# Kernel tuning notes

Hardware: AMD Instinct MI355X
Metric: run time of the kernel (lower is better)

## Reference

```python
import jax, jax.numpy as jnp
import numpy as np

OUT_FEATURES = 11008
IN_FEATURES = 4096
PACKED_LEN = OUT_FEATURES * IN_FEATURES // 4  # 4 ternary vals per byte, 2 bits each


def setup_inputs() -> dict:
    key = jax.random.key(0)
    k1, k2, k3 = jax.random.split(key, 3)
    x = jax.random.normal(k1, (4, 1024, IN_FEATURES), dtype=jnp.float32)
    packed_weight = jax.random.randint(k2, (PACKED_LEN,), 0, 256, dtype=jnp.int32)
    weight_scale = jax.random.uniform(k3, (1,), dtype=jnp.float32)
    return {"x": x, "packed_weight": packed_weight, "weight_scale": weight_scale}


def _dequantize_weight(packed_weight, weight_scale):
    shifts = jnp.arange(0, 8, 2, dtype=jnp.int32)          # [4]
    q = ((packed_weight[:, None] >> shifts) & 3) - 1        # [P, 4]
    q = q.reshape(OUT_FEATURES, IN_FEATURES).astype(jnp.float32)
    return q * weight_scale.reshape(())                      # dequantize


def reference(x, packed_weight, weight_scale):
    w = _dequantize_weight(packed_weight, weight_scale)      # [out, in]
    # F.linear: y = x @ w.T  (bias=False)
    return jnp.einsum('bsi,oi->bso', x, w)
```

## Files before the change

### kernel.cpp

```cpp
#include <hip/hip_runtime.h>
#include <hip/hip_bf16.h>

#define OUT_F 11008
#define IN_F  4096
#define M_DIM 4096

typedef __attribute__((ext_vector_type(8))) short bf16x8;
typedef __attribute__((ext_vector_type(4))) float f32x4;
typedef __attribute__((ext_vector_type(8))) unsigned short us8;

__device__ __forceinline__ unsigned short f2bf_rne(float f) {
    unsigned u = __builtin_bit_cast(unsigned, f);
    u += 0x7fffu + ((u >> 16) & 1u);
    return (unsigned short)(u >> 16);
}

__global__ void cvt_x_kernel(const float* __restrict__ x,
                             unsigned short* __restrict__ xb) {
    size_t i = ((size_t)blockIdx.x * blockDim.x + threadIdx.x) * 8;
    float4 a = *(const float4*)(x + i);
    float4 b = *(const float4*)(x + i + 4);
    us8 o;
    o[0] = f2bf_rne(a.x); o[1] = f2bf_rne(a.y);
    o[2] = f2bf_rne(a.z); o[3] = f2bf_rne(a.w);
    o[4] = f2bf_rne(b.x); o[5] = f2bf_rne(b.y);
    o[6] = f2bf_rne(b.z); o[7] = f2bf_rne(b.w);
    *(us8*)(xb + i) = o;
}

__global__ void unpack_w_kernel(const int* __restrict__ pw,
                                unsigned short* __restrict__ wb) {
    size_t i = (size_t)blockIdx.x * blockDim.x + threadIdx.x;
    int4 v = ((const int4*)pw)[i];
    const unsigned long long LUT = 0x40003F800000BF80ull;
    us8 o0, o1;
#pragma unroll
    for (int j = 0; j < 4; j++) {
        o0[j]     = (unsigned short)(LUT >> (((v.x >> (2 * j)) & 3) * 16));
        o0[4 + j] = (unsigned short)(LUT >> (((v.y >> (2 * j)) & 3) * 16));
        o1[j]     = (unsigned short)(LUT >> (((v.z >> (2 * j)) & 3) * 16));
        o1[4 + j] = (unsigned short)(LUT >> (((v.w >> (2 * j)) & 3) * 16));
    }
    ((us8*)wb)[i * 2]     = o0;
    ((us8*)wb)[i * 2 + 1] = o1;
}

__global__ __launch_bounds__(256) void gemm_kernel(
    const unsigned short* __restrict__ A,
    const unsigned short* __restrict__ B,
    float* __restrict__ C,
    const float* __restrict__ scale_ptr) {
    constexpr int K = IN_F;
    constexpr int N = OUT_F;
    constexpr int NB_N = 86;

    __shared__ unsigned short sA[128 * 32];
    __shared__ unsigned short sB[128 * 32];

    const int tid  = threadIdx.x;
    const int wave = tid >> 6;
    const int lane = tid & 63;

    const int lin = blockIdx.y * gridDim.x + blockIdx.x;
    const int grp = lin >> 8;
    const int rem = lin & 255;
    const int gw  = (grp * 8 + 8 <= NB_N) ? 8 : (NB_N - grp * 8);
    const int bn  = grp * 8 + rem % gw;
    const int bm  = rem / gw;

    const int wm = (wave >> 1) * 64;
    const int wn = (wave & 1) * 64;

    const int srow = lane >> 2;
    const int sseg = (lane & 3) ^ ((lane >> 3) & 3);
    const int scol = sseg * 8;

    const unsigned short* Ag = A + (size_t)bm * 128 * K;
    const unsigned short* Bg = B + (size_t)bn * 128 * K;

    f32x4 acc[4][4];
#pragma unroll
    for (int i = 0; i < 4; i++)
#pragma unroll
        for (int j = 0; j < 4; j++) acc[i][j] = (f32x4){0.f, 0.f, 0.f, 0.f};

    const int quad = lane >> 4;
    const int mrow = lane & 15;
    const int sw   = quad ^ ((mrow >> 1) & 3);

    for (int k0 = 0; k0 < K; k0 += 32) {
        __syncthreads();
#pragma unroll
        for (int c = 0; c < 2; c++) {
            const int chunk = wave * 2 + c;
            const int row = chunk * 16 + srow;
            __builtin_amdgcn_global_load_lds(
                (const __attribute__((address_space(1))) void*)(Ag + (size_t)row * K + k0 + scol),
                (__attribute__((address_space(3))) void*)(sA + chunk * 512),
                16, 0, 0);
        }
#pragma unroll
        for (int c = 0; c < 2; c++) {
            const int chunk = wave * 2 + c;
            const int row = chunk * 16 + srow;
            __builtin_amdgcn_global_load_lds(
                (const __attribute__((address_space(1))) void*)(Bg + (size_t)row * K + k0 + scol),
                (__attribute__((address_space(3))) void*)(sB + chunk * 512),
                16, 0, 0);
        }
        __syncthreads();

        bf16x8 af[4], bfg[4];
#pragma unroll
        for (int t = 0; t < 4; t++) {
            const int ra = wm + t * 16 + mrow;
            const int rb = wn + t * 16 + mrow;
            af[t]  = *(const bf16x8*)(sA + (ra * 4 + sw) * 8);
            bfg[t] = *(const bf16x8*)(sB + (rb * 4 + sw) * 8);
        }
#pragma unroll
        for (int i = 0; i < 4; i++)
#pragma unroll
            for (int j = 0; j < 4; j++)
                acc[i][j] = __builtin_amdgcn_mfma_f32_16x16x32_bf16(
                    af[i], bfg[j], acc[i][j], 0, 0, 0);
    }

    const float scale = *scale_ptr;
    float* Cg = C + (size_t)bm * 128 * N + (size_t)bn * 128;
#pragma unroll
    for (int i = 0; i < 4; i++) {
#pragma unroll
        for (int j = 0; j < 4; j++) {
#pragma unroll
            for (int r = 0; r < 4; r++) {
                const int row = wm + i * 16 + quad * 4 + r;
                const int col = wn + j * 16 + mrow;
                Cg[(size_t)row * N + col] = acc[i][j][r] * scale;
            }
        }
    }
}

extern "C" void kernel_launch(void* const* d_in, const int* in_sizes, int n_in,
                              void* d_out, int out_size, void* d_ws, size_t ws_size,
                              hipStream_t stream) {
    const float* x   = (const float*)d_in[0];
    const int* pw    = (const int*)d_in[1];
    const float* wsc = (const float*)d_in[2];

    float* out = (float*)d_out;

    unsigned short* xb = (unsigned short*)d_ws;
    unsigned short* wb = (unsigned short*)((char*)d_ws + (size_t)M_DIM * IN_F * 2);

    cvt_x_kernel<<<8192, 256, 0, stream>>>(x, xb);

    unpack_w_kernel<<<11008, 256, 0, stream>>>(pw, wb);

    gemm_kernel<<<dim3(86, 32), 256, 0, stream>>>(xb, wb, out, wsc);
}
```

Measured before the change: 675.5 us.

## Use 256x256 tiles with double-buffered LDS pipeline and XCD-aware block mapping

Rewrites the GEMM to use 256x256 block tiles with 8 waves (each 128x64), a K step of 64 split into two 32-wide halves, and double-buffered LDS. Global-to-LDS prefetch of the next tile is interleaved with MFMA phases through explicit vmcnt/lgkmcnt waits, barriers and setprio. Blocks are remapped on a 1D grid so that each XCD works on neighbouring M rows, which is meant to improve L2 reuse. The aim is to raise arithmetic intensity and hide load latency, at the cost of more registers (128 accumulator floats per lane) and a more fragile hand-tuned schedule.

```diff
diff --git a/kernel.cpp b/kernel.cpp
--- a/kernel.cpp
+++ b/kernel.cpp
@@ -45,97 +45,156 @@
     ((us8*)wb)[i * 2 + 1] = o1;
 }
 
-__global__ __launch_bounds__(256) void gemm_kernel(
+#define LGKM0() do { asm volatile("s_waitcnt lgkmcnt(0)" ::: "memory"); \
+                     __builtin_amdgcn_sched_barrier(0); } while (0)
+#define VMCNT(n) do { asm volatile("s_waitcnt vmcnt(" #n ")" ::: "memory"); \
+                      __builtin_amdgcn_sched_barrier(0); } while (0)
+
+__global__ __launch_bounds__(512, 2) void gemm_kernel(
     const unsigned short* __restrict__ A,
     const unsigned short* __restrict__ B,
     float* __restrict__ C,
     const float* __restrict__ scale_ptr) {
-    constexpr int K = IN_F;
-    constexpr int N = OUT_F;
-    constexpr int NB_N = 86;
-
-    __shared__ unsigned short sA[128 * 32];
-    __shared__ unsigned short sB[128 * 32];
+    constexpr int K  = IN_F;
+    constexpr int N  = OUT_F;
+    constexpr int NT = K / 64;
+
+    __shared__ unsigned short lds[2][2][2][256][32];
 
     const int tid  = threadIdx.x;
     const int wave = tid >> 6;
     const int lane = tid & 63;
-
-    const int lin = blockIdx.y * gridDim.x + blockIdx.x;
-    const int grp = lin >> 8;
-    const int rem = lin & 255;
-    const int gw  = (grp * 8 + 8 <= NB_N) ? 8 : (NB_N - grp * 8);
-    const int bn  = grp * 8 + rem % gw;
-    const int bm  = rem / gw;
-
-    const int wm = (wave >> 1) * 64;
-    const int wn = (wave & 1) * 64;
-
-    const int srow = lane >> 2;
-    const int sseg = (lane & 3) ^ ((lane >> 3) & 3);
-    const int scol = sseg * 8;
-
-    const unsigned short* Ag = A + (size_t)bm * 128 * K;
-    const unsigned short* Bg = B + (size_t)bn * 128 * K;
-
-    f32x4 acc[4][4];
-#pragma unroll
-    for (int i = 0; i < 4; i++)
-#pragma unroll
-        for (int j = 0; j < 4; j++) acc[i][j] = (f32x4){0.f, 0.f, 0.f, 0.f};
-
     const int quad = lane >> 4;
     const int mrow = lane & 15;
     const int sw   = quad ^ ((mrow >> 1) & 3);
 
-    for (int k0 = 0; k0 < K; k0 += 32) {
-        __syncthreads();
-#pragma unroll
-        for (int c = 0; c < 2; c++) {
+    const int srow = lane >> 2;
+    const int sseg = (lane & 3) ^ ((lane >> 3) & 3);
+
+    const int lin = blockIdx.x;
+    const int xcd = lin & 7;
+    const int q   = lin >> 3;
+    const int bm  = xcd * 2 + q / 43;
+    const int bn  = q % 43;
+
+    const int wm = (wave >> 2) * 128;
+    const int wn = (wave & 3) * 64;
+
+    const unsigned short* Ag = A + (size_t)bm * 256 * K;
+    const unsigned short* Bg = B + (size_t)bn * 256 * K;
+
+    f32x4 acc[8][4];
+#pragma unroll
+    for (int i = 0; i < 8; i++)
+#pragma unroll
+        for (int j = 0; j < 4; j++) acc[i][j] = (f32x4){0.f, 0.f, 0.f, 0.f};
+
+    auto STAGE = [&](int mat, int nb, int h, int kbase) {
+#pragma unroll
+        for (int c = 0; c < 2; ++c) {
             const int chunk = wave * 2 + c;
-            const int row = chunk * 16 + srow;
+            const int grow  = chunk * 16 + srow;
+            const unsigned short* src =
+                (mat ? Bg : Ag) + (size_t)grow * K + kbase + sseg * 8;
             __builtin_amdgcn_global_load_lds(
-                (const __attribute__((address_space(1))) void*)(Ag + (size_t)row * K + k0 + scol),
-                (__attribute__((address_space(3))) void*)(sA + chunk * 512),
+                (const __attribute__((address_space(1))) void*)src,
+                (__attribute__((address_space(3))) void*)
+                    (&lds[nb][mat][h][0][0] + chunk * 512),
                 16, 0, 0);
         }
-#pragma unroll
-        for (int c = 0; c < 2; c++) {
-            const int chunk = wave * 2 + c;
-            const int row = chunk * 16 + srow;
-            __builtin_amdgcn_global_load_lds(
-                (const __attribute__((address_space(1))) void*)(Bg + (size_t)row * K + k0 + scol),
-                (__attribute__((address_space(3))) void*)(sB + chunk * 512),
-                16, 0, 0);
-        }
-        __syncthreads();
-
-        bf16x8 af[4], bfg[4];
-#pragma unroll
-        for (int t = 0; t < 4; t++) {
-            const int ra = wm + t * 16 + mrow;
-            const int rb = wn + t * 16 + mrow;
-            af[t]  = *(const bf16x8*)(sA + (ra * 4 + sw) * 8);
-            bfg[t] = *(const bf16x8*)(sB + (rb * 4 + sw) * 8);
-        }
-#pragma unroll
-        for (int i = 0; i < 4; i++)
-#pragma unroll
-            for (int j = 0; j < 4; j++)
-                acc[i][j] = __builtin_amdgcn_mfma_f32_16x16x32_bf16(
-                    af[i], bfg[j], acc[i][j], 0, 0, 0);
+    };
+
+    STAGE(0, 0, 0, 0);
+    STAGE(1, 0, 0, 0);
+    STAGE(0, 0, 1, 32);
+    STAGE(1, 0, 1, 32);
+    VMCNT(4);
+    __builtin_amdgcn_s_barrier();
+
+    bf16x8 a[8], b0, b1, b2, b3;
+
+#pragma unroll 2
+    for (int kt = 0; kt < NT; ++kt) {
+        const int  buf  = kt & 1;
+        const int  nbuf = buf ^ 1;
+        const bool pf   = (kt + 1 < NT);
+        const int  kn   = (kt + 1) * 64;
+
+#pragma unroll
+        for (int t = 0; t < 8; ++t)
+            a[t] = *(const bf16x8*)&lds[buf][0][0][wm + t * 16 + mrow][sw * 8];
+        b0 = *(const bf16x8*)&lds[buf][1][0][wn +  0 + mrow][sw * 8];
+        b1 = *(const bf16x8*)&lds[buf][1][0][wn + 16 + mrow][sw * 8];
+        if (pf) STAGE(0, nbuf, 0, kn);
+        __builtin_amdgcn_s_barrier();
+        LGKM0();
+        __builtin_amdgcn_s_setprio(1);
+#pragma unroll
+        for (int t = 0; t < 8; ++t) {
+            acc[t][0] = __builtin_amdgcn_mfma_f32_16x16x32_bf16(a[t], b0, acc[t][0], 0, 0, 0);
+            acc[t][1] = __builtin_amdgcn_mfma_f32_16x16x32_bf16(a[t], b1, acc[t][1], 0, 0, 0);
+        }
+        __builtin_amdgcn_s_setprio(0);
+        __builtin_amdgcn_s_barrier();
+
+        b2 = *(const bf16x8*)&lds[buf][1][0][wn + 32 + mrow][sw * 8];
+        b3 = *(const bf16x8*)&lds[buf][1][0][wn + 48 + mrow][sw * 8];
+        if (pf) STAGE(1, nbuf, 0, kn);
+        __builtin_amdgcn_s_barrier();
+        LGKM0();
+        __builtin_amdgcn_s_setprio(1);
+#pragma unroll
+        for (int t = 0; t < 8; ++t) {
+            acc[t][2] = __builtin_amdgcn_mfma_f32_16x16x32_bf16(a[t], b2, acc[t][2], 0, 0, 0);
+            acc[t][3] = __builtin_amdgcn_mfma_f32_16x16x32_bf16(a[t], b3, acc[t][3], 0, 0, 0);
+        }
+        __builtin_amdgcn_s_setprio(0);
+        if (pf) { VMCNT(4); } else { VMCNT(0); }
+        __builtin_amdgcn_s_barrier();
+
+#pragma unroll
+        for (int t = 0; t < 8; ++t)
+            a[t] = *(const bf16x8*)&lds[buf][0][1][wm + t * 16 + mrow][sw * 8];
+        b0 = *(const bf16x8*)&lds[buf][1][1][wn +  0 + mrow][sw * 8];
+        b1 = *(const bf16x8*)&lds[buf][1][1][wn + 16 + mrow][sw * 8];
+        if (pf) STAGE(0, nbuf, 1, kn + 32);
+        __builtin_amdgcn_s_barrier();
+        LGKM0();
+        __builtin_amdgcn_s_setprio(1);
+#pragma unroll
+        for (int t = 0; t < 8; ++t) {
+            acc[t][0] = __builtin_amdgcn_mfma_f32_16x16x32_bf16(a[t], b0, acc[t][0], 0, 0, 0);
+            acc[t][1] = __builtin_amdgcn_mfma_f32_16x16x32_bf16(a[t], b1, acc[t][1], 0, 0, 0);
+        }
+        __builtin_amdgcn_s_setprio(0);
+        __builtin_amdgcn_s_barrier();
+
+        b2 = *(const bf16x8*)&lds[buf][1][1][wn + 32 + mrow][sw * 8];
+        b3 = *(const bf16x8*)&lds[buf][1][1][wn + 48 + mrow][sw * 8];
+        if (pf) STAGE(1, nbuf, 1, kn + 32);
+        __builtin_amdgcn_s_barrier();
+        LGKM0();
+        __builtin_amdgcn_s_setprio(1);
+#pragma unroll
+        for (int t = 0; t < 8; ++t) {
+            acc[t][2] = __builtin_amdgcn_mfma_f32_16x16x32_bf16(a[t], b2, acc[t][2], 0, 0, 0);
+            acc[t][3] = __builtin_amdgcn_mfma_f32_16x16x32_bf16(a[t], b3, acc[t][3], 0, 0, 0);
+        }
+        __builtin_amdgcn_s_setprio(0);
+        if (pf) { VMCNT(4); }
+        __builtin_amdgcn_s_barrier();
     }
 
     const float scale = *scale_ptr;
-    float* Cg = C + (size_t)bm * 128 * N + (size_t)bn * 128;
-#pragma unroll
-    for (int i = 0; i < 4; i++) {
-#pragma unroll
-        for (int j = 0; j < 4; j++) {
-#pragma unroll
-            for (int r = 0; r < 4; r++) {
-                const int row = wm + i * 16 + quad * 4 + r;
-                const int col = wn + j * 16 + mrow;
+    float* Cg = C + (size_t)(bm * 256 + wm) * N + bn * 256 + wn;
+#pragma unroll
+    for (int i = 0; i < 8; ++i) {
+#pragma unroll
+        for (int j = 0; j < 4; ++j) {
+#pragma unroll
+            for (int r = 0; r < 4; ++r) {
+                const int row = i * 16 + quad * 4 + r;
+                const int col = j * 16 + mrow;
                 Cg[(size_t)row * N + col] = acc[i][j][r] * scale;
             }
         }
@@ -158,5 +217,5 @@
 
     unpack_w_kernel<<<11008, 256, 0, stream>>>(pw, wb);
 
-    gemm_kernel<<<dim3(86, 32), 256, 0, stream>>>(xb, wb, out, wsc);
-}
+    gemm_kernel<<<688, 512, 0, stream>>>(xb, wb, out, wsc);
+}
```

Result: faster. 587.6 us (-13.0%).
